# Optimization experiments

Measured on AMD Instinct MI355X. Metric: run time of the kernel, lower is better.

The kernel has to match this reference:

```python
import jax, jax.numpy as jnp
import numpy as np

EMB = 1024
HEADS = 16
HEAD_DIM = EMB // HEADS
SCALE = 1.0 / np.sqrt(HEAD_DIM)


def setup_inputs() -> dict:
    key = jax.random.key(0)
    ks = jax.random.split(key, 11)
    B, L, E = 4, 2048, EMB
    s = 1.0 / np.sqrt(E)
    inp = {
        "Q": jax.random.normal(ks[0], (B, L, E), jnp.float32),
        "K": jax.random.normal(ks[1], (B, L, E), jnp.float32),
        "V": jax.random.normal(ks[2], (B, L, E), jnp.float32),
        "WQ": jax.random.normal(ks[3], (E, E), jnp.float32) * s,
        "bQ": jax.random.normal(ks[4], (E,), jnp.float32) * s,
        "WK": jax.random.normal(ks[5], (E, E), jnp.float32) * s,
        "bK": jax.random.normal(ks[6], (E,), jnp.float32) * s,
        "WV": jax.random.normal(ks[7], (E, E), jnp.float32) * s,
        "bV": jax.random.normal(ks[8], (E,), jnp.float32) * s,
        "WO": jax.random.normal(ks[9], (E, E), jnp.float32) * s,
        "bO": jax.random.normal(ks[10], (E,), jnp.float32) * s,
    }
    return inp


def reference(Q, K, V, WQ, bQ, WK, bK, WV, bV, WO, bO):
    B, L, E = Q.shape
    # linear projections (torch Linear stores W as [out,in]; here W is [in,out])
    q = Q @ WQ + bQ
    k = K @ WK + bK
    v = V @ WV + bV
    # split heads: [B, H, L, D]
    q = q.reshape(B, L, HEADS, HEAD_DIM).transpose(0, 2, 1, 3)
    k = k.reshape(B, L, HEADS, HEAD_DIM).transpose(0, 2, 1, 3)
    v = v.reshape(B, L, HEADS, HEAD_DIM).transpose(0, 2, 1, 3)
    scores = jnp.einsum("bhqd,bhkd->bhqk", q, k) * SCALE
    # causal mask (mask=True): -inf above diagonal
    causal = jnp.tril(jnp.ones((L, L), dtype=bool))
    scores = jnp.where(causal, scores, -jnp.inf)
    probs = jax.nn.softmax(scores, axis=-1)
    out = jnp.einsum("bhqk,bhkd->bhqd", probs, v)  # [B,H,L,D]
    out = out.transpose(0, 2, 1, 3).reshape(B, L, E)  # concat heads
    return out @ WO + bO
```

## Files before the change

kernel.cpp:

```cpp
#include <hip/hip_runtime.h>
#include <hip/hip_bf16.h>

#define BB 4
#define HH 16
#define LL 2048
#define DD 64
#define EE 1024
#define MM (BB*LL)
#define SCL 0.125f
#define L2E 1.44269504f

using bf16   = __hip_bfloat16;
using bf16x8 = __attribute__((ext_vector_type(8))) __bf16;
using s16x4  = __attribute__((ext_vector_type(4))) short;
using f32x4  = __attribute__((ext_vector_type(4))) float;
using u32x4  = __attribute__((ext_vector_type(4))) unsigned int;
typedef unsigned int u32;

__device__ __forceinline__ bf16x8 ld8(const bf16* p){ return *(const bf16x8*)p; }
__device__ __forceinline__ bf16x8 ld8(const float* p){
  u32x4 a = *(const u32x4*)p;
  u32x4 b = *(const u32x4*)(p + 4);
  union { bf16x8 v; unsigned short s[8]; } r;
#pragma unroll
  for (int i = 0; i < 4; i++) r.s[i]     = (unsigned short)((a[i] + 0x7FFFu + ((a[i] >> 16) & 1u)) >> 16);
#pragma unroll
  for (int i = 0; i < 4; i++) r.s[i + 4] = (unsigned short)((b[i] + 0x7FFFu + ((b[i] >> 16) & 1u)) >> 16);
  return r.v;
}
__device__ __forceinline__ float ldf(const bf16* p){ return __bfloat162float(*p); }
__device__ __forceinline__ float ldf(const float* p){ return *p; }
__device__ __forceinline__ bf16 to_b(bf16 v){ return v; }
__device__ __forceinline__ bf16 to_b(float v){ return __float2bfloat16(v); }

__device__ __forceinline__ bf16x8 scl8(bf16x8 v){
  union { bf16x8 v; unsigned short s[8]; } a, r;
  a.v = v;
#pragma unroll
  for (int i = 0; i < 8; i++) {
    bf16 b; *(unsigned short*)&b = a.s[i];
    bf16 c = __float2bfloat16(__bfloat162float(b) * 0.125f);
    r.s[i] = *(unsigned short*)&c;
  }
  return r.v;
}

__device__ __forceinline__ void async16(const bf16* g, bf16* l) {
  __builtin_amdgcn_global_load_lds((const __attribute__((address_space(1))) u32*)g,
                                   (__attribute__((address_space(3))) u32*)l, 16, 0, 0);
}

__global__ __launch_bounds__(256) void detect_dtype(const unsigned int* __restrict__ w,
                                                    int* __restrict__ flag) {
  __shared__ int cnt[256];
  int tid = threadIdx.x;
  int c = 0;
  for (int i = 0; i < 16; i++) {
    unsigned u = w[tid * 16 + i];
    unsigned e = (u >> 7) & 0xFF;
    c += (e >= 100 && e <= 140) ? 1 : 0;
  }
  cnt[tid] = c;
  __syncthreads();
  for (int s = 128; s > 0; s >>= 1) {
    if (tid < s) cnt[tid] += cnt[tid + s];
    __syncthreads();
  }
  if (tid == 0) *flag = (cnt[0] > 2048) ? 1 : 0;
}

__global__ __launch_bounds__(256) void convert_in(
    const void* __restrict__ X0, const void* __restrict__ X1, const void* __restrict__ X2,
    bf16* __restrict__ Y0, bf16* __restrict__ Y1, bf16* __restrict__ Y2,
    const int* __restrict__ flag) {
  int z = blockIdx.z;
  const void* X = (z == 0) ? X0 : (z == 1) ? X1 : X2;
  bf16* Y       = (z == 0) ? Y0 : (z == 1) ? Y1 : Y2;
  size_t idx = ((size_t)blockIdx.x * 256 + threadIdx.x) * 8;
  if (*flag) *(bf16x8*)(Y + idx) = *(const bf16x8*)((const bf16*)X + idx);
  else       *(bf16x8*)(Y + idx) = ld8((const float*)X + idx);
}

template<typename T>
__device__ __forceinline__ void tr_body(const T* __restrict__ W, bf16* __restrict__ Wt,
                                        bf16 (*t)[33]) {
  int tx = threadIdx.x, ty = threadIdx.y;
  int x = blockIdx.x * 32 + tx;
  for (int r = 0; r < 4; r++)
    t[ty + r * 8][tx] = to_b(W[(blockIdx.y * 32 + ty + r * 8) * EE + x]);
  __syncthreads();
  int x2 = blockIdx.y * 32 + tx;
  for (int r = 0; r < 4; r++)
    Wt[(blockIdx.x * 32 + ty + r * 8) * EE + x2] = t[tx][ty + r * 8];
}

__global__ __launch_bounds__(256) void transpose_w4(
    const void* __restrict__ W0, const void* __restrict__ W1,
    const void* __restrict__ W2, const void* __restrict__ W3,
    bf16* __restrict__ T0, bf16* __restrict__ T1,
    bf16* __restrict__ T2, bf16* __restrict__ T3,
    const int* __restrict__ flag) {
  __shared__ bf16 t[32][33];
  int z = blockIdx.z;
  const void* W = (z == 0) ? W0 : (z == 1) ? W1 : (z == 2) ? W2 : W3;
  bf16* Wt      = (z == 0) ? T0 : (z == 1) ? T1 : (z == 2) ? T2 : T3;
  if (*flag) tr_body<bf16>((const bf16*)W, Wt, t);
  else       tr_body<float>((const float*)W, Wt, t);
}

#define TILE_A (128 * 32)
template<typename TIO, bool SW>
__device__ void gemm_body(const bf16* __restrict__ A, const bf16* __restrict__ Bt,
                          const TIO* __restrict__ bias, void* __restrict__ Cv,
                          int mode, bf16* As, bf16* Bs) {
  constexpr int K = EE;
  int tid = threadIdx.x;
  int lane = tid & 63, w = tid >> 6;
  int l16 = lane & 15, quad = lane >> 4;
  int linear = blockIdx.x + 8 * blockIdx.y;
  int xcd = linear & 7;
  int slot = linear >> 3;
  int m0 = (xcd * 8 + (slot & 7)) * 128;
  int n0 = (slot >> 3) * 128;
  int mw = (w & 1) * 64;
  int nw = (w >> 1) * 64;
  int lr = lane >> 2;
  int lc = (lane & 3) * 8;

  f32x4 acc[4][4] = {};

  auto stage = [&](bf16* Ad, bf16* Bd, int k0) {
#pragma unroll
    for (int s = 0; s < 2; s++) {
      int r = w * 32 + s * 16;
      async16(A  + (size_t)(m0 + r + lr) * K + k0 + lc, Ad + r * 32);
      async16(Bt + (size_t)(n0 + r + lr) * K + k0 + lc, Bd + r * 32);
    }
  };

  auto compute = [&](const bf16* Ab, const bf16* Bb) {
    bf16x8 af[4], bfr[4];
#pragma unroll
    for (int t = 0; t < 4; t++) {
      af[t]  = *(const bf16x8*)(Ab + (mw + t * 16 + l16) * 32 + quad * 8);
      bfr[t] = *(const bf16x8*)(Bb + (nw + t * 16 + l16) * 32 + quad * 8);
    }
#pragma unroll
    for (int mt = 0; mt < 4; mt++)
#pragma unroll
      for (int nt = 0; nt < 4; nt++) {
        if (SW)
          acc[mt][nt] = __builtin_amdgcn_mfma_f32_16x16x32_bf16(bfr[nt], af[mt], acc[mt][nt], 0, 0, 0);
        else
          acc[mt][nt] = __builtin_amdgcn_mfma_f32_16x16x32_bf16(af[mt], bfr[nt], acc[mt][nt], 0, 0, 0);
      }
  };

  stage(As, Bs, 0);
  asm volatile("s_waitcnt vmcnt(0)" ::: "memory");
  __builtin_amdgcn_s_barrier();
  asm volatile("" ::: "memory");

#pragma unroll 1
  for (int t = 0; t < K / 32; t += 2) {
    stage(As + TILE_A, Bs + TILE_A, t * 32 + 32);
    compute(As, Bs);
    asm volatile("s_waitcnt vmcnt(0)" ::: "memory");
    __builtin_amdgcn_s_barrier();
    asm volatile("" ::: "memory");
    if (t + 2 < K / 32)
      stage(As, Bs, t * 32 + 64);
    compute(As + TILE_A, Bs + TILE_A);
    asm volatile("s_waitcnt vmcnt(0)" ::: "memory");
    __builtin_amdgcn_s_barrier();
    asm volatile("" ::: "memory");
  }

  if (SW) {
#pragma unroll
    for (int mt = 0; mt < 4; mt++) {
      int row = m0 + mw + mt * 16 + l16;
#pragma unroll
      for (int nt = 0; nt < 4; nt++) {
        int colb = n0 + nw + nt * 16 + quad * 4;
        f32x4 v = acc[mt][nt];
        if (mode == 0) {
          union { s16x4 v4; bf16 e[4]; } u;
#pragma unroll
          for (int i = 0; i < 4; i++) u.e[i] = __float2bfloat16(v[i] + ldf(bias + colb + i));
          *(s16x4*)((bf16*)Cv + (size_t)row * EE + colb) = u.v4;
        } else {
          if constexpr (__is_same(TIO, bf16)) {
            union { s16x4 v4; bf16 e[4]; } u;
#pragma unroll
            for (int i = 0; i < 4; i++) u.e[i] = __float2bfloat16(v[i] + ldf(bias + colb + i));
            *(s16x4*)((bf16*)Cv + (size_t)row * EE + colb) = u.v4;
          } else {
            f32x4 fv;
#pragma unroll
            for (int i = 0; i < 4; i++) fv[i] = v[i] + ldf(bias + colb + i);
            *(f32x4*)((float*)Cv + (size_t)row * EE + colb) = fv;
          }
        }
      }
    }
  } else {
#pragma unroll
    for (int nt = 0; nt < 4; nt++) {
      int col = n0 + nw + nt * 16 + l16;
      float bv = ldf(bias + col);
      int hh = col >> 6, d = col & 63;
#pragma unroll
      for (int mt = 0; mt < 4; mt++) {
        f32x4 v = acc[mt][nt];
        int rowb = m0 + mw + mt * 16 + quad * 4;
        int b = rowb >> 11, l0 = rowb & 2047;
        union { s16x4 p; bf16 e[4]; } u;
#pragma unroll
        for (int i = 0; i < 4; i++) u.e[i] = __float2bfloat16(v[i] + bv);
        *(s16x4*)((bf16*)Cv + ((size_t)(b * HH + hh) * DD + d) * LL + l0) = u.p;
      }
    }
  }
}

__global__ __launch_bounds__(256) void qkv_gemm(
    const bf16* __restrict__ Qc, const bf16* __restrict__ Kc, const bf16* __restrict__ Vc,
    const bf16* __restrict__ WQt, const bf16* __restrict__ WKt, const bf16* __restrict__ WVt,
    const void* __restrict__ bQ, const void* __restrict__ bK, const void* __restrict__ bV,
    bf16* __restrict__ qo, bf16* __restrict__ ko, bf16* __restrict__ vo,
    const int* __restrict__ flag) {
  __shared__ __align__(16) bf16 As[2 * TILE_A];
  __shared__ __align__(16) bf16 Bs[2 * TILE_A];
  int z = blockIdx.z;
  const bf16* A    = (z == 0) ? Qc  : (z == 1) ? Kc  : Vc;
  const bf16* Bt   = (z == 0) ? WQt : (z == 1) ? WKt : WVt;
  const void* bb   = (z == 0) ? bQ  : (z == 1) ? bK  : bV;
  bf16* C          = (z == 0) ? qo  : (z == 1) ? ko  : vo;
  if (z == 2) {
    if (*flag) gemm_body<bf16,  false>(A, Bt, (const bf16*)bb,  C, 2, As, Bs);
    else       gemm_body<float, false>(A, Bt, (const float*)bb, C, 2, As, Bs);
  } else {
    if (*flag) gemm_body<bf16,  true>(A, Bt, (const bf16*)bb,  C, 0, As, Bs);
    else       gemm_body<float, true>(A, Bt, (const float*)bb, C, 0, As, Bs);
  }
}

__global__ __launch_bounds__(256) void out_gemm(const bf16* __restrict__ A,
                                                const bf16* __restrict__ WOt,
                                                const void* __restrict__ bO,
                                                void* __restrict__ C,
                                                const int* __restrict__ flag) {
  __shared__ __align__(16) bf16 As[2 * TILE_A];
  __shared__ __align__(16) bf16 Bs[2 * TILE_A];
  if (*flag) gemm_body<bf16,  true>(A, WOt, (const bf16*)bO,  C, 3, As, Bs);
  else       gemm_body<float, true>(A, WOt, (const float*)bO, C, 3, As, Bs);
}

__global__ __launch_bounds__(256) void attn(const bf16* __restrict__ qg,
                                            const bf16* __restrict__ kg,
                                            const bf16* __restrict__ vg,
                                            bf16* __restrict__ outg) {
  __shared__ __align__(16) bf16 Ks[2][64 * 64];
  __shared__ __align__(16) bf16 Vs[2][64 * 64];
  int linear = blockIdx.x + 16 * blockIdx.y;
  int xcd = linear & 7;
  int slot = linear >> 3;
  int bh = xcd * 8 + (slot & 7);
  int pb = slot >> 3;
  int tid = threadIdx.x;
  int w = tid >> 6, lane = tid & 63, l16 = lane & 15, quad = lane >> 4;
  int b = bh >> 4, hh = bh & 15;

  const bf16* qp = qg + (size_t)b * LL * EE + hh * DD;
  const bf16* kp = kg + (size_t)b * LL * EE + hh * DD;
  const bf16* vp = vg + (size_t)bh * DD * LL;
  const f32x4 z4 = {};
  int x7 = l16 & 7;
  int gb = (lane & 7) ^ (lane >> 3);

  for (int half = 0; half < 2; half++) {
    int tile = half ? (31 - pb) : pb;
    int qrow0 = tile * 64 + w * 16;
    int q = qrow0 + l16;
    bf16x8 bq0 = scl8(*(const bf16x8*)(qp + (size_t)q * EE + quad * 8));
    bf16x8 bq1 = scl8(*(const bf16x8*)(qp + (size_t)q * EE + 32 + quad * 8));

    float l = 0.f;
    f32x4 o[4] = {};
    int kend = tile + 1;

    const bf16* kP[2];
    const bf16* vP[2];
#pragma unroll
    for (int t = 0; t < 2; t++) {
      int r = w * 16 + t * 8 + (lane >> 3);
      kP[t] = kp + (size_t)r * EE + gb * 8;
      vP[t] = vp + (size_t)r * LL + gb * 8;
    }

    __syncthreads();
#pragma unroll
    for (int t = 0; t < 2; t++) {
      int R = w * 16 + t * 8;
      async16(kP[t], &Ks[0][R * 64]);
      async16(vP[t], &Vs[0][R * 64]);
      kP[t] += (size_t)64 * EE;
      vP[t] += 64;
    }

    auto body = [&](int kb, const bf16* Kb, const bf16* Vb, bf16* KsN, bf16* VsN) {
      int kbase = kb * 64;
      __syncthreads();
      if (kb + 1 < kend) {
#pragma unroll
        for (int t = 0; t < 2; t++) {
          int R = w * 16 + t * 8;
          async16(kP[t], KsN + R * 64);
          async16(vP[t], VsN + R * 64);
          kP[t] += (size_t)64 * EE;
          vP[t] += 64;
        }
      }

      f32x4 s[4];
      __builtin_amdgcn_s_setprio(1);
#pragma unroll
      for (int kt = 0; kt < 4; kt++) {
        int row = kt * 16 + l16;
        bf16x8 kf0 = *(const bf16x8*)(Kb + row * 64 + (quad ^ x7) * 8);
        bf16x8 kf1 = *(const bf16x8*)(Kb + row * 64 + ((quad + 4) ^ x7) * 8);
        s[kt] = __builtin_amdgcn_mfma_f32_16x16x32_bf16(kf0, bq0, z4, 0, 0, 0);
        s[kt] = __builtin_amdgcn_mfma_f32_16x16x32_bf16(kf1, bq1, s[kt], 0, 0, 0);
      }
      __builtin_amdgcn_s_setprio(0);
#if __has_builtin(__builtin_amdgcn_mfma_f32_16x16x16bf16_1k)
      s16x4 vf[4][4];
#pragma unroll
      for (int j = 0; j < 4; j++)
#pragma unroll
        for (int kt = 0; kt < 4; kt++)
          vf[j][kt] = *(const s16x4*)(Vb + (j * 16 + l16) * 64 +
                                      ((kt * 2 + (quad >> 1)) ^ x7) * 8 + (quad & 1) * 4);
#endif
      float p[16];
      if (kbase + 63 <= qrow0) {
#pragma unroll
        for (int kt = 0; kt < 4; kt++)
#pragma unroll
          for (int i = 0; i < 4; i++) {
            float pv = exp2f(s[kt][i] * L2E);
            p[kt * 4 + i] = pv;
            l += pv;
          }
      } else {
        int rel = q - kbase - quad * 4;
#pragma unroll
        for (int kt = 0; kt < 4; kt++)
#pragma unroll
          for (int i = 0; i < 4; i++) {
            float pv = (kt * 16 + i <= rel) ? exp2f(s[kt][i] * L2E) : 0.f;
            p[kt * 4 + i] = pv;
            l += pv;
          }
      }
      union { s16x4 v4; unsigned u[2]; } pk[4];
#pragma unroll
      for (int kt = 0; kt < 4; kt++) {
        __hip_bfloat162 h0 = __float22bfloat162_rn(float2{p[kt * 4 + 0], p[kt * 4 + 1]});
        __hip_bfloat162 h1 = __float22bfloat162_rn(float2{p[kt * 4 + 2], p[kt * 4 + 3]});
        __builtin_memcpy(&pk[kt].u[0], &h0, 4);
        __builtin_memcpy(&pk[kt].u[1], &h1, 4);
      }
#if __has_builtin(__builtin_amdgcn_mfma_f32_16x16x16bf16_1k)
      __builtin_amdgcn_s_setprio(1);
#pragma unroll
      for (int kt = 0; kt < 4; kt++)
#pragma unroll
        for (int j = 0; j < 4; j++)
          o[j] = __builtin_amdgcn_mfma_f32_16x16x16bf16_1k(vf[j][kt], pk[kt].v4, o[j], 0, 0, 0);
      __builtin_amdgcn_s_setprio(0);
#else
#pragma unroll
      for (int c = 0; c < 2; c++) {
        union { bf16x8 v8; unsigned u[4]; } bfr;
#pragma unroll
        for (int r = 0; r < 4; r++) {
          int key = c * 32 + quad * 8 + 2 * r;
          int srcl = (((key >> 2) & 3) << 4) + l16;
          unsigned v0 = __shfl((int)pk[2 * c].u[r & 1], srcl, 64);
          unsigned v1 = __shfl((int)pk[2 * c + 1].u[r & 1], srcl, 64);
          bfr.u[r] = (quad < 2) ? v0 : v1;
        }
        __builtin_amdgcn_s_setprio(1);
#pragma unroll
        for (int j = 0; j < 4; j++) {
          bf16x8 vfr = *(const bf16x8*)(Vb + (j * 16 + l16) * 64 + ((c * 4 + quad) ^ x7) * 8);
          o[j] = __builtin_amdgcn_mfma_f32_16x16x32_bf16(vfr, bfr.v8, o[j], 0, 0, 0);
        }
        __builtin_amdgcn_s_setprio(0);
      }
#endif
    };

    int kb = 0;
    for (;;) {
      body(kb, &Ks[0][0], &Vs[0][0], &Ks[1][0], &Vs[1][0]);
      if (++kb >= kend) break;
      body(kb, &Ks[1][0], &Vs[1][0], &Ks[0][0], &Vs[0][0]);
      if (++kb >= kend) break;
    }

    l += __shfl_xor(l, 16);
    l += __shfl_xor(l, 32);

    float inv = 1.0f / l;
#pragma unroll
    for (int j = 0; j < 4; j++) {
      union { s16x4 v4; bf16 e[4]; } u;
#pragma unroll
      for (int i = 0; i < 4; i++) u.e[i] = __float2bfloat16(o[j][i] * inv);
      *(s16x4*)(outg + (size_t)(b * LL + q) * EE + hh * DD + j * 16 + quad * 4) = u.v4;
    }
  }
}

extern "C" void kernel_launch(void* const* d_in, const int* in_sizes, int n_in,
                              void* d_out, int out_size, void* d_ws, size_t ws_size,
                              hipStream_t stream) {
  const void* Q   = d_in[0];
  const void* Kin = d_in[1];
  const void* V   = d_in[2];
  const void* WQ  = d_in[3];
  const void* bQ  = d_in[4];
  const void* WK  = d_in[5];
  const void* bK  = d_in[6];
  const void* WV  = d_in[7];
  const void* bV  = d_in[8];
  const void* WO  = d_in[9];
  const void* bO  = d_in[10];

  int* flag = (int*)d_ws;
  bf16* base = (bf16*)((char*)d_ws + 256);
  bf16* wqt  = base;
  bf16* wkt  = wqt + (size_t)EE * EE;
  bf16* wvt  = wkt + (size_t)EE * EE;
  bf16* wot  = wvt + (size_t)EE * EE;
  bf16* Qc   = wot + (size_t)EE * EE;
  bf16* Kc   = Qc  + (size_t)MM * EE;
  bf16* Vc   = Kc  + (size_t)MM * EE;
  bf16* qws  = Vc  + (size_t)MM * EE;
  bf16* kws  = qws + (size_t)MM * EE;
  bf16* vws  = kws + (size_t)MM * EE;
  bf16* aout = vws + (size_t)MM * EE;

  detect_dtype<<<1, 256, 0, stream>>>((const unsigned int*)WQ, flag);

  convert_in<<<dim3(MM * EE / 8 / 256, 1, 3), 256, 0, stream>>>(Q, Kin, V, Qc, Kc, Vc, flag);

  transpose_w4<<<dim3(32, 32, 4), dim3(32, 8), 0, stream>>>(
      WQ, WK, WV, WO, wqt, wkt, wvt, wot, flag);

  qkv_gemm<<<dim3(8, 64, 3), 256, 0, stream>>>(
      Qc, Kc, Vc, wqt, wkt, wvt, bQ, bK, bV, qws, kws, vws, flag);

  attn<<<dim3(16, 64), 256, 0, stream>>>(qws, kws, vws, aout);

  out_gemm<<<dim3(8, 64), 256, 0, stream>>>(aout, wot, bO, d_out, flag);
}
```

Baseline: 366.7 us.

## Triple-buffer K/V tiles in attention with two-ahead async prefetch

Grows the attention K/V shared-memory staging from two buffers to three and issues async loads two tiles ahead. The top-of-iteration __syncthreads is replaced by an explicit vmcnt wait plus barrier at the end of each iteration, so a tile's load has a full extra iteration to land before it is used. This is meant to hide global-load latency behind the MFMA work. In exchange LDS use grows by half (48KB per block), which may reduce occupancy, and correctness now depends on the hand-counted vmcnt values.

```diff
diff --git a/kernel.cpp b/kernel.cpp
--- a/kernel.cpp
+++ b/kernel.cpp
@@ -261,8 +261,8 @@
                                             const bf16* __restrict__ kg,
                                             const bf16* __restrict__ vg,
                                             bf16* __restrict__ outg) {
-  __shared__ __align__(16) bf16 Ks[2][64 * 64];
-  __shared__ __align__(16) bf16 Vs[2][64 * 64];
+  __shared__ __align__(16) bf16 Ks[3][64 * 64];
+  __shared__ __align__(16) bf16 Vs[3][64 * 64];
   int linear = blockIdx.x + 16 * blockIdx.y;
   int xcd = linear & 7;
   int slot = linear >> 3;
@@ -299,29 +299,32 @@
       vP[t] = vp + (size_t)r * LL + gb * 8;
     }
 
+    auto stageKV = [&](bf16* Kd, bf16* Vd) {
+#pragma unroll
+      for (int t = 0; t < 2; t++) {
+        int R = w * 16 + t * 8;
+        async16(kP[t], Kd + R * 64);
+        async16(vP[t], Vd + R * 64);
+        kP[t] += (size_t)64 * EE;
+        vP[t] += 64;
+      }
+    };
+
     __syncthreads();
-#pragma unroll
-    for (int t = 0; t < 2; t++) {
-      int R = w * 16 + t * 8;
-      async16(kP[t], &Ks[0][R * 64]);
-      async16(vP[t], &Vs[0][R * 64]);
-      kP[t] += (size_t)64 * EE;
-      vP[t] += 64;
-    }
+    stageKV(&Ks[0][0], &Vs[0][0]);
+    if (kend > 1) {
+      stageKV(&Ks[1][0], &Vs[1][0]);
+      asm volatile("s_waitcnt vmcnt(4)" ::: "memory");
+    } else {
+      asm volatile("s_waitcnt vmcnt(0)" ::: "memory");
+    }
+    __builtin_amdgcn_s_barrier();
+    asm volatile("" ::: "memory");
 
     auto body = [&](int kb, const bf16* Kb, const bf16* Vb, bf16* KsN, bf16* VsN) {
       int kbase = kb * 64;
-      __syncthreads();
-      if (kb + 1 < kend) {
-#pragma unroll
-        for (int t = 0; t < 2; t++) {
-          int R = w * 16 + t * 8;
-          async16(kP[t], KsN + R * 64);
-          async16(vP[t], VsN + R * 64);
-          kP[t] += (size_t)64 * EE;
-          vP[t] += 64;
-        }
-      }
+      bool pf = (kb + 2 < kend);
+      if (pf) stageKV(KsN, VsN);
 
       f32x4 s[4];
       __builtin_amdgcn_s_setprio(1);
@@ -401,14 +404,17 @@
         __builtin_amdgcn_s_setprio(0);
       }
 #endif
+      if (pf) asm volatile("s_waitcnt vmcnt(4)" ::: "memory");
+      else    asm volatile("s_waitcnt vmcnt(0)" ::: "memory");
+      __builtin_amdgcn_s_barrier();
+      asm volatile("" ::: "memory");
     };
 
     int kb = 0;
     for (;;) {
-      body(kb, &Ks[0][0], &Vs[0][0], &Ks[1][0], &Vs[1][0]);
-      if (++kb >= kend) break;
-      body(kb, &Ks[1][0], &Vs[1][0], &Ks[0][0], &Vs[0][0]);
-      if (++kb >= kend) break;
+      body(kb, &Ks[0][0], &Vs[0][0], &Ks[2][0], &Vs[2][0]); if (++kb >= kend) break;
+      body(kb, &Ks[1][0], &Vs[1][0], &Ks[0][0], &Vs[0][0]); if (++kb >= kend) break;
+      body(kb, &Ks[2][0], &Vs[2][0], &Ks[1][0], &Vs[1][0]); if (++kb >= kend) break;
     }
 
     l += __shfl_xor(l, 16);
```

New measurement: 367.6 us. No clear change (+0.2%).

## Process two 64-row query tiles per wave to reuse staged K/V blocks

Applied to the files above, without the earlier changes.

Each attention block now handles a 128-row query strip: every wave owns two 16-row query fragments 64 rows apart, so each K/V tile loaded into shared memory feeds twice as many MFMAs. The grid is halved to 512 blocks, with causal pairing over 16 strips instead of 32 tiles. This cuts K/V global and LDS traffic per unit of work, at the cost of more registers (two sets of accumulators and scores), fewer blocks to fill the CUs, and some wasted masked work on the lower fragment's diagonal tile.

```diff
diff --git a/kernel.cpp b/kernel.cpp
--- a/kernel.cpp
+++ b/kernel.cpp
@@ -263,11 +263,11 @@
                                             bf16* __restrict__ outg) {
   __shared__ __align__(16) bf16 Ks[2][64 * 64];
   __shared__ __align__(16) bf16 Vs[2][64 * 64];
-  int linear = blockIdx.x + 16 * blockIdx.y;
+  int linear = blockIdx.x + 8 * blockIdx.y;
   int xcd = linear & 7;
   int slot = linear >> 3;
   int bh = xcd * 8 + (slot & 7);
-  int pb = slot >> 3;
+  int pp = slot >> 3;
   int tid = threadIdx.x;
   int w = tid >> 6, lane = tid & 63, l16 = lane & 15, quad = lane >> 4;
   int b = bh >> 4, hh = bh & 15;
@@ -280,15 +280,19 @@
   int gb = (lane & 7) ^ (lane >> 3);
 
   for (int half = 0; half < 2; half++) {
-    int tile = half ? (31 - pb) : pb;
-    int qrow0 = tile * 64 + w * 16;
-    int q = qrow0 + l16;
-    bf16x8 bq0 = scl8(*(const bf16x8*)(qp + (size_t)q * EE + quad * 8));
-    bf16x8 bq1 = scl8(*(const bf16x8*)(qp + (size_t)q * EE + 32 + quad * 8));
-
-    float l = 0.f;
-    f32x4 o[4] = {};
-    int kend = tile + 1;
+    int st = half ? (15 - pp) : pp;
+    int qrow0 = st * 128 + w * 16;
+    int q0 = qrow0 + l16;
+    bf16x8 bq[2][2];
+#pragma unroll
+    for (int f = 0; f < 2; f++) {
+      bq[f][0] = scl8(*(const bf16x8*)(qp + (size_t)(q0 + f * 64) * EE + quad * 8));
+      bq[f][1] = scl8(*(const bf16x8*)(qp + (size_t)(q0 + f * 64) * EE + 32 + quad * 8));
+    }
+
+    float lsum[2] = {0.f, 0.f};
+    f32x4 o[2][4] = {};
+    int kend = 2 * st + 2;
 
     const bf16* kP[2];
     const bf16* vP[2];
@@ -299,39 +303,36 @@
       vP[t] = vp + (size_t)r * LL + gb * 8;
     }
 
+    auto stageKV = [&](bf16* Kd, bf16* Vd) {
+#pragma unroll
+      for (int t = 0; t < 2; t++) {
+        int R = w * 16 + t * 8;
+        async16(kP[t], Kd + R * 64);
+        async16(vP[t], Vd + R * 64);
+        kP[t] += (size_t)64 * EE;
+        vP[t] += 64;
+      }
+    };
+
     __syncthreads();
-#pragma unroll
-    for (int t = 0; t < 2; t++) {
-      int R = w * 16 + t * 8;
-      async16(kP[t], &Ks[0][R * 64]);
-      async16(vP[t], &Vs[0][R * 64]);
-      kP[t] += (size_t)64 * EE;
-      vP[t] += 64;
-    }
+    stageKV(&Ks[0][0], &Vs[0][0]);
 
     auto body = [&](int kb, const bf16* Kb, const bf16* Vb, bf16* KsN, bf16* VsN) {
       int kbase = kb * 64;
       __syncthreads();
-      if (kb + 1 < kend) {
-#pragma unroll
-        for (int t = 0; t < 2; t++) {
-          int R = w * 16 + t * 8;
-          async16(kP[t], KsN + R * 64);
-          async16(vP[t], VsN + R * 64);
-          kP[t] += (size_t)64 * EE;
-          vP[t] += 64;
-        }
-      }
-
-      f32x4 s[4];
+      if (kb + 1 < kend) stageKV(KsN, VsN);
+
+      f32x4 s[2][4];
       __builtin_amdgcn_s_setprio(1);
 #pragma unroll
       for (int kt = 0; kt < 4; kt++) {
         int row = kt * 16 + l16;
         bf16x8 kf0 = *(const bf16x8*)(Kb + row * 64 + (quad ^ x7) * 8);
         bf16x8 kf1 = *(const bf16x8*)(Kb + row * 64 + ((quad + 4) ^ x7) * 8);
-        s[kt] = __builtin_amdgcn_mfma_f32_16x16x32_bf16(kf0, bq0, z4, 0, 0, 0);
-        s[kt] = __builtin_amdgcn_mfma_f32_16x16x32_bf16(kf1, bq1, s[kt], 0, 0, 0);
+        s[0][kt] = __builtin_amdgcn_mfma_f32_16x16x32_bf16(kf0, bq[0][0], z4, 0, 0, 0);
+        s[0][kt] = __builtin_amdgcn_mfma_f32_16x16x32_bf16(kf1, bq[0][1], s[0][kt], 0, 0, 0);
+        s[1][kt] = __builtin_amdgcn_mfma_f32_16x16x32_bf16(kf0, bq[1][0], z4, 0, 0, 0);
+        s[1][kt] = __builtin_amdgcn_mfma_f32_16x16x32_bf16(kf1, bq[1][1], s[1][kt], 0, 0, 0);
       }
       __builtin_amdgcn_s_setprio(0);
 #if __has_builtin(__builtin_amdgcn_mfma_f32_16x16x16bf16_1k)
@@ -343,64 +344,68 @@
           vf[j][kt] = *(const s16x4*)(Vb + (j * 16 + l16) * 64 +
                                       ((kt * 2 + (quad >> 1)) ^ x7) * 8 + (quad & 1) * 4);
 #endif
-      float p[16];
-      if (kbase + 63 <= qrow0) {
+#pragma unroll
+      for (int f = 0; f < 2; f++) {
+        int qr = qrow0 + f * 64;
+        float p[16];
+        if (kbase + 63 <= qr) {
+#pragma unroll
+          for (int kt = 0; kt < 4; kt++)
+#pragma unroll
+            for (int i = 0; i < 4; i++) {
+              float pv = exp2f(s[f][kt][i] * L2E);
+              p[kt * 4 + i] = pv;
+              lsum[f] += pv;
+            }
+        } else {
+          int rel = q0 + f * 64 - kbase - quad * 4;
+#pragma unroll
+          for (int kt = 0; kt < 4; kt++)
+#pragma unroll
+            for (int i = 0; i < 4; i++) {
+              float pv = (kt * 16 + i <= rel) ? exp2f(s[f][kt][i] * L2E) : 0.f;
+              p[kt * 4 + i] = pv;
+              lsum[f] += pv;
+            }
+        }
+        union { s16x4 v4; unsigned u[2]; } pk[4];
+#pragma unroll
+        for (int kt = 0; kt < 4; kt++) {
+          __hip_bfloat162 h0 = __float22bfloat162_rn(float2{p[kt * 4 + 0], p[kt * 4 + 1]});
+          __hip_bfloat162 h1 = __float22bfloat162_rn(float2{p[kt * 4 + 2], p[kt * 4 + 3]});
+          __builtin_memcpy(&pk[kt].u[0], &h0, 4);
+          __builtin_memcpy(&pk[kt].u[1], &h1, 4);
+        }
+#if __has_builtin(__builtin_amdgcn_mfma_f32_16x16x16bf16_1k)
+        __builtin_amdgcn_s_setprio(1);
 #pragma unroll
         for (int kt = 0; kt < 4; kt++)
 #pragma unroll
-          for (int i = 0; i < 4; i++) {
-            float pv = exp2f(s[kt][i] * L2E);
-            p[kt * 4 + i] = pv;
-            l += pv;
+          for (int j = 0; j < 4; j++)
+            o[f][j] = __builtin_amdgcn_mfma_f32_16x16x16bf16_1k(vf[j][kt], pk[kt].v4, o[f][j], 0, 0, 0);
+        __builtin_amdgcn_s_setprio(0);
+#else
+#pragma unroll
+        for (int c = 0; c < 2; c++) {
+          union { bf16x8 v8; unsigned u[4]; } bfr;
+#pragma unroll
+          for (int r = 0; r < 4; r++) {
+            int key = c * 32 + quad * 8 + 2 * r;
+            int srcl = (((key >> 2) & 3) << 4) + l16;
+            unsigned v0 = __shfl((int)pk[2 * c].u[r & 1], srcl, 64);
+            unsigned v1 = __shfl((int)pk[2 * c + 1].u[r & 1], srcl, 64);
+            bfr.u[r] = (quad < 2) ? v0 : v1;
           }
-      } else {
-        int rel = q - kbase - quad * 4;
-#pragma unroll
-        for (int kt = 0; kt < 4; kt++)
-#pragma unroll
-          for (int i = 0; i < 4; i++) {
-            float pv = (kt * 16 + i <= rel) ? exp2f(s[kt][i] * L2E) : 0.f;
-            p[kt * 4 + i] = pv;
-            l += pv;
+          __builtin_amdgcn_s_setprio(1);
+#pragma unroll
+          for (int j = 0; j < 4; j++) {
+            bf16x8 vfr = *(const bf16x8*)(Vb + (j * 16 + l16) * 64 + ((c * 4 + quad) ^ x7) * 8);
+            o[f][j] = __builtin_amdgcn_mfma_f32_16x16x32_bf16(vfr, bfr.v8, o[f][j], 0, 0, 0);
           }
-      }
-      union { s16x4 v4; unsigned u[2]; } pk[4];
-#pragma unroll
-      for (int kt = 0; kt < 4; kt++) {
-        __hip_bfloat162 h0 = __float22bfloat162_rn(float2{p[kt * 4 + 0], p[kt * 4 + 1]});
-        __hip_bfloat162 h1 = __float22bfloat162_rn(float2{p[kt * 4 + 2], p[kt * 4 + 3]});
-        __builtin_memcpy(&pk[kt].u[0], &h0, 4);
-        __builtin_memcpy(&pk[kt].u[1], &h1, 4);
-      }
-#if __has_builtin(__builtin_amdgcn_mfma_f32_16x16x16bf16_1k)
-      __builtin_amdgcn_s_setprio(1);
-#pragma unroll
-      for (int kt = 0; kt < 4; kt++)
-#pragma unroll
-        for (int j = 0; j < 4; j++)
-          o[j] = __builtin_amdgcn_mfma_f32_16x16x16bf16_1k(vf[j][kt], pk[kt].v4, o[j], 0, 0, 0);
-      __builtin_amdgcn_s_setprio(0);
-#else
-#pragma unroll
-      for (int c = 0; c < 2; c++) {
-        union { bf16x8 v8; unsigned u[4]; } bfr;
-#pragma unroll
-        for (int r = 0; r < 4; r++) {
-          int key = c * 32 + quad * 8 + 2 * r;
-          int srcl = (((key >> 2) & 3) << 4) + l16;
-          unsigned v0 = __shfl((int)pk[2 * c].u[r & 1], srcl, 64);
-          unsigned v1 = __shfl((int)pk[2 * c + 1].u[r & 1], srcl, 64);
-          bfr.u[r] = (quad < 2) ? v0 : v1;
+          __builtin_amdgcn_s_setprio(0);
         }
-        __builtin_amdgcn_s_setprio(1);
-#pragma unroll
-        for (int j = 0; j < 4; j++) {
-          bf16x8 vfr = *(const bf16x8*)(Vb + (j * 16 + l16) * 64 + ((c * 4 + quad) ^ x7) * 8);
-          o[j] = __builtin_amdgcn_mfma_f32_16x16x32_bf16(vfr, bfr.v8, o[j], 0, 0, 0);
-        }
-        __builtin_amdgcn_s_setprio(0);
-      }
 #endif
+      }
     };
 
     int kb = 0;
@@ -411,16 +416,19 @@
       if (++kb >= kend) break;
     }
 
-    l += __shfl_xor(l, 16);
-    l += __shfl_xor(l, 32);
-
-    float inv = 1.0f / l;
-#pragma unroll
-    for (int j = 0; j < 4; j++) {
-      union { s16x4 v4; bf16 e[4]; } u;
-#pragma unroll
-      for (int i = 0; i < 4; i++) u.e[i] = __float2bfloat16(o[j][i] * inv);
-      *(s16x4*)(outg + (size_t)(b * LL + q) * EE + hh * DD + j * 16 + quad * 4) = u.v4;
+#pragma unroll
+    for (int f = 0; f < 2; f++) {
+      float l = lsum[f];
+      l += __shfl_xor(l, 16);
+      l += __shfl_xor(l, 32);
+      float inv = 1.0f / l;
+#pragma unroll
+      for (int j = 0; j < 4; j++) {
+        union { s16x4 v4; bf16 e[4]; } u;
+#pragma unroll
+        for (int i = 0; i < 4; i++) u.e[i] = __float2bfloat16(o[f][j][i] * inv);
+        *(s16x4*)(outg + (size_t)(b * LL + q0 + f * 64) * EE + hh * DD + j * 16 + quad * 4) = u.v4;
+      }
     }
   }
 }
@@ -464,7 +472,7 @@
   qkv_gemm<<<dim3(8, 64, 3), 256, 0, stream>>>(
       Qc, Kc, Vc, wqt, wkt, wvt, bQ, bK, bV, qws, kws, vws, flag);
 
-  attn<<<dim3(16, 64), 256, 0, stream>>>(qws, kws, vws, aout);
+  attn<<<dim3(8, 64), 256, 0, stream>>>(qws, kws, vws, aout);
 
   out_gemm<<<dim3(8, 64), 256, 0, stream>>>(aout, wot, bO, d_out, flag);
 }
```

New measurement: 389.1 us. +6.1%, slower.
